# Performance work log

Hardware: AMD Instinct MI355X
Metric: run time of the kernel (lower is better)

Reference implementation:

```python
import jax, jax.numpy as jnp
import numpy as np

B, CQ, CKV, H, W = 8, 256, 512, 64, 64
HKV, WKV = 32, 32
DQK = CQ // 8  # 32


def setup_inputs() -> dict:
    key = jax.random.key(0)
    ks = jax.random.split(key, 9)
    s = 0.05
    return {
        "query": jax.random.normal(ks[0], (B, CQ, H, W), jnp.float32),
        "key_value": jax.random.normal(ks[1], (B, CKV, HKV, WKV), jnp.float32),
        "Wq": jax.random.normal(ks[2], (DQK, CQ), jnp.float32) * s,
        "bq": jax.random.normal(ks[3], (DQK,), jnp.float32) * s,
        "Wk": jax.random.normal(ks[4], (DQK, CKV), jnp.float32) * s,
        "bk": jax.random.normal(ks[5], (DQK,), jnp.float32) * s,
        "Wv": jax.random.normal(ks[6], (CQ, CKV), jnp.float32) * s,
        "bv": jax.random.normal(ks[7], (CQ,), jnp.float32) * s,
        "gamma": jax.random.normal(ks[8], (1,), jnp.float32) * 0.5,
    }


def reference(query, key_value, Wq, bq, Wk, bk, Wv, bv, gamma):
    b, cq, h, w = query.shape
    n = h * w
    # bilinear resize of key_value to query's spatial size (align_corners=False
    # half-pixel convention, matching torch F.interpolate and jax.image.resize)
    kv = jax.image.resize(key_value, (b, key_value.shape[1], h, w), method="bilinear")
    # 1x1 convs are channel contractions
    q = jnp.einsum("bchw,dc->bdhw", query, Wq) + bq[None, :, None, None]   # [B,DQK,H,W]
    k = jnp.einsum("bchw,dc->bdhw", kv, Wk) + bk[None, :, None, None]      # [B,DQK,H,W]
    v = jnp.einsum("bchw,dc->bdhw", kv, Wv) + bv[None, :, None, None]      # [B,CQ,H,W]
    qf = q.reshape(b, -1, n)   # [B,DQK,N]
    kf = k.reshape(b, -1, n)   # [B,DQK,N]
    vf = v.reshape(b, -1, n)   # [B,CQ,N]
    energy = jnp.einsum("bdn,bdm->bnm", qf, kf)        # [B,N,N]
    attention = jax.nn.softmax(energy, axis=-1)
    out = jnp.einsum("bnm,bcm->bcn", attention, vf)     # [B,CQ,N]
    out = out.reshape(b, cq, h, w)
    return gamma[0] * out + query
```

## Files before the change

### kernel.cpp

```cpp
#include <hip/hip_runtime.h>

#define B_ 8
#define CQ_ 256
#define CKV_ 512
#define N_ 4096
#define DQK_ 32

typedef __bf16 bf16;
typedef __bf16 bf16x4 __attribute__((ext_vector_type(4)));
typedef __bf16 bf16x8 __attribute__((ext_vector_type(8)));
typedef float f32x4 __attribute__((ext_vector_type(4)));

__global__ void k_convert_w(const float* __restrict__ Wq, const float* __restrict__ Wk,
                            const float* __restrict__ Wv,
                            bf16* __restrict__ wq, bf16* __restrict__ wk, bf16* __restrict__ wv) {
    int i = blockIdx.x * 256 + threadIdx.x;
    if (i < 8192) wq[i] = (bf16)Wq[i];
    else if (i < 24576) wk[i - 8192] = (bf16)Wk[i - 8192];
    else if (i < 155648) wv[i - 24576] = (bf16)Wv[i - 24576];
}

__global__ __launch_bounds__(256) void k_resize(const float* __restrict__ kv, bf16* __restrict__ kvr) {
    const int yo = blockIdx.x;
    const int b  = blockIdx.y;
    const int tid = threadIdx.x;
    __shared__ float r0[64][33];
    __shared__ float r1[64][33];
    int ty = yo >> 1;
    int y0, y1; float wy0, wy1;
    if ((yo & 1) == 0) { y0 = ty > 0 ? ty - 1 : 0; y1 = ty; wy0 = 0.25f; wy1 = 0.75f; }
    else               { y0 = ty; y1 = ty < 31 ? ty + 1 : 31; wy0 = 0.75f; wy1 = 0.25f; }
    const int u_loc = tid & 63;
    const int xo_base = tid >> 6;
    for (int uc = 0; uc < CKV_; uc += 64) {
        __syncthreads();
        for (int i = 0; i < 8; ++i) {
            int idx = tid + i * 256;
            int u = idx >> 5, x = idx & 31;
            const float* src = kv + ((size_t)b * CKV_ + uc + u) * 1024 + x;
            r0[u][x] = src[y0 * 32];
            r1[u][x] = src[y1 * 32];
        }
        __syncthreads();
        for (int i = 0; i < 16; ++i) {
            int xo = xo_base + i * 4;
            int tx = xo >> 1;
            int xa, xb; float wxa, wxb;
            if ((xo & 1) == 0) { xa = tx > 0 ? tx - 1 : 0; xb = tx; wxa = 0.25f; wxb = 0.75f; }
            else               { xa = tx; xb = tx < 31 ? tx + 1 : 31; wxa = 0.75f; wxb = 0.25f; }
            float v0 = wxa * r0[u_loc][xa] + wxb * r0[u_loc][xb];
            float v1 = wxa * r1[u_loc][xa] + wxb * r1[u_loc][xb];
            float val = wy0 * v0 + wy1 * v1;
            kvr[((size_t)b * N_ + yo * 64 + xo) * CKV_ + uc + u_loc] = (bf16)val;
        }
    }
}

__global__ __launch_bounds__(256) void k_proj_q_fused(const float* __restrict__ query,
                                                      const bf16* __restrict__ W,
                                                      const float* __restrict__ bias,
                                                      bf16* __restrict__ qTb) {
    __shared__ bf16 tile[64][264];
    const int n0 = blockIdx.x * 64;
    const int b  = blockIdx.y;
    const int tid = threadIdx.x;
    const int xi = tid & 15, c0 = tid >> 4;
    for (int pass = 0; pass < 16; ++pass) {
        int c = c0 + pass * 16;
        const float4 v = *(const float4*)(query + ((size_t)b * CQ_ + c) * N_ + n0 + xi * 4);
        tile[xi * 4 + 0][c] = (bf16)v.x;
        tile[xi * 4 + 1][c] = (bf16)v.y;
        tile[xi * 4 + 2][c] = (bf16)v.z;
        tile[xi * 4 + 3][c] = (bf16)v.w;
    }
    __syncthreads();
    const int w = tid >> 6, lane = tid & 63;
    const int l16 = lane & 15, quad = lane >> 4;
    const int ct = w & 1, nh = w >> 1;
    f32x4 acc[2];
    acc[0] = (f32x4){0.f, 0.f, 0.f, 0.f}; acc[1] = (f32x4){0.f, 0.f, 0.f, 0.f};
    const bf16* aptr = W + (ct * 16 + l16) * CQ_ + quad * 8;
#pragma unroll
    for (int ks = 0; ks < 8; ++ks) {
        bf16x8 af = *(const bf16x8*)(aptr + ks * 32);
        for (int j = 0; j < 2; ++j) {
            bf16x8 bfv = *(const bf16x8*)&tile[nh * 32 + j * 16 + l16][ks * 32 + quad * 8];
            acc[j] = __builtin_amdgcn_mfma_f32_16x16x32_bf16(af, bfv, acc[j], 0, 0, 0);
        }
    }
    for (int j = 0; j < 2; ++j)
        for (int r = 0; r < 4; ++r) {
            int d = ct * 16 + quad * 4 + r;
            int n = n0 + nh * 32 + j * 16 + l16;
            qTb[((size_t)b * N_ + n) * DQK_ + d] = (bf16)(acc[j][r] + bias[d]);
        }
}

__global__ __launch_bounds__(256) void k_proj_k(const bf16* __restrict__ W,
                                                const float* __restrict__ bias,
                                                const bf16* __restrict__ Bm,
                                                bf16* __restrict__ outT) {
    const int mb = blockIdx.x * 128;
    const int b  = blockIdx.y;
    const int tid = threadIdx.x;
    const int w = tid >> 6, lane = tid & 63;
    const int l16 = lane & 15, quad = lane >> 4;
    const int ct = w & 1;
    const int mhalf = (w >> 1) * 64;
    f32x4 acc[4];
    for (int j = 0; j < 4; ++j) acc[j] = (f32x4){0.f, 0.f, 0.f, 0.f};
    const bf16* aptr  = W + (ct * 16 + l16) * CKV_ + quad * 8;
    const bf16* bbase = Bm + ((size_t)b * N_ + mb + mhalf) * CKV_ + quad * 8;
#pragma unroll
    for (int ks = 0; ks < 16; ++ks) {
        bf16x8 af = *(const bf16x8*)(aptr + ks * 32);
        for (int j = 0; j < 4; ++j) {
            bf16x8 bfv = *(const bf16x8*)(bbase + (size_t)(j * 16 + l16) * CKV_ + ks * 32);
            acc[j] = __builtin_amdgcn_mfma_f32_16x16x32_bf16(af, bfv, acc[j], 0, 0, 0);
        }
    }
    for (int j = 0; j < 4; ++j)
        for (int r = 0; r < 4; ++r) {
            int d = ct * 16 + quad * 4 + r;
            int m = mb + mhalf + j * 16 + l16;
            outT[((size_t)b * N_ + m) * DQK_ + d] = (bf16)(acc[j][r] + bias[d]);
        }
}

__global__ __launch_bounds__(256) void k_proj_v(const bf16* __restrict__ W,
                                                const float* __restrict__ bias,
                                                const bf16* __restrict__ Bm,
                                                bf16* __restrict__ vout) {
    const int mb = blockIdx.x * 64;
    const int b  = blockIdx.y;
    const int tid = threadIdx.x;
    const int w = tid >> 6, lane = tid & 63;
    const int l16 = lane & 15, quad = lane >> 4;
    f32x4 acc[4][4];
    for (int i = 0; i < 4; ++i) for (int j = 0; j < 4; ++j) acc[i][j] = (f32x4){0.f, 0.f, 0.f, 0.f};
    const bf16* bbase = Bm + ((size_t)b * N_ + mb) * CKV_ + quad * 8;
#pragma unroll 4
    for (int ks = 0; ks < 16; ++ks) {
        bf16x8 bfv[4];
        for (int j = 0; j < 4; ++j)
            bfv[j] = *(const bf16x8*)(bbase + (size_t)(j * 16 + l16) * CKV_ + ks * 32);
        for (int i = 0; i < 4; ++i) {
            bf16x8 af = *(const bf16x8*)(W + (size_t)((w * 4 + i) * 16 + l16) * CKV_ + ks * 32 + quad * 8);
            for (int j = 0; j < 4; ++j)
                acc[i][j] = __builtin_amdgcn_mfma_f32_16x16x32_bf16(af, bfv[j], acc[i][j], 0, 0, 0);
        }
    }
    for (int i = 0; i < 4; ++i)
        for (int r = 0; r < 4; ++r) {
            int c = (w * 4 + i) * 16 + quad * 4 + r;
            float bvs = bias[c];
            for (int j = 0; j < 4; ++j) {
                int m = mb + j * 16 + l16;
                vout[((size_t)b * CQ_ + c) * N_ + m] = (bf16)(acc[i][j][r] + bvs);
            }
        }
}

__global__ __launch_bounds__(256) void k_flash(const bf16* __restrict__ qT,
                                               const bf16* __restrict__ kT,
                                               const bf16* __restrict__ vv,
                                               const float* __restrict__ query,
                                               const float* __restrict__ gamma,
                                               float* __restrict__ out) {
    __shared__ bf16 P[2][64][72];
    __shared__ float linvs[64];
    const int b  = blockIdx.y;
    const int n0 = blockIdx.x * 64;
    const int tid = threadIdx.x;
    const int w = tid >> 6, lane = tid & 63;
    const int l16 = lane & 15, quad = lane >> 4;
    const int swz = l16 & 3;

    const bf16x8 qfrag = *(const bf16x8*)(qT + ((size_t)b * N_ + n0 + w * 16 + l16) * DQK_ + quad * 8);

    f32x4 acc[4][4];
    for (int i = 0; i < 4; ++i) for (int j = 0; j < 4; ++j) acc[i][j] = (f32x4){0.f, 0.f, 0.f, 0.f};
    f32x4 lsum = (f32x4){0.f, 0.f, 0.f, 0.f};

    const bf16* kbase = kT + (size_t)b * N_ * DQK_;
    const bf16* vbase = vv + ((size_t)b * CQ_ + w * 64) * N_;

    bf16x8 kf[4];
    for (int im = 0; im < 4; ++im)
        kf[im] = *(const bf16x8*)(kbase + (size_t)(im * 16 + l16) * DQK_ + quad * 8);

    for (int mt = 0; mt < 64; ++mt) {
        const int m0 = mt * 64;
        bf16 (* __restrict__ Pb)[72] = P[mt & 1];
        for (int im = 0; im < 4; ++im) {
            f32x4 s = __builtin_amdgcn_mfma_f32_16x16x32_bf16(kf[im], qfrag,
                                                              (f32x4){0.f, 0.f, 0.f, 0.f}, 0, 0, 0);
            bf16x4 pk;
            for (int r = 0; r < 4; ++r) {
                float p = __expf(s[r]);
                lsum[r] += p;
                pk[r] = (bf16)p;
            }
            *(bf16x4*)&Pb[w * 16 + l16][((im ^ swz) << 4) + quad * 4] = pk;
        }
        bf16x8 vf[2][4];
        for (int ks = 0; ks < 2; ++ks)
            for (int i = 0; i < 4; ++i)
                vf[ks][i] = *(const bf16x8*)(vbase + (size_t)(i * 16 + l16) * N_ + m0 + ks * 32 + quad * 8);
        const int m1 = (mt + 1 < 64 ? mt + 1 : 0) * 64;
        bf16x8 kn[4];
        for (int im = 0; im < 4; ++im)
            kn[im] = *(const bf16x8*)(kbase + (size_t)(m1 + im * 16 + l16) * DQK_ + quad * 8);
        __syncthreads();
        for (int ks = 0; ks < 2; ++ks) {
            bf16x8 pf[4];
            for (int j = 0; j < 4; ++j)
                pf[j] = *(const bf16x8*)&Pb[j * 16 + l16]
                            [((((ks << 1) | (quad >> 1)) ^ swz) << 4) + ((quad & 1) << 3)];
            for (int i = 0; i < 4; ++i)
                for (int j = 0; j < 4; ++j)
                    acc[i][j] = __builtin_amdgcn_mfma_f32_16x16x32_bf16(vf[ks][i], pf[j], acc[i][j], 0, 0, 0);
        }
        for (int im = 0; im < 4; ++im) kf[im] = kn[im];
    }
    float s = (lsum[0] + lsum[1]) + (lsum[2] + lsum[3]);
    s += __shfl_xor(s, 16);
    s += __shfl_xor(s, 32);
    if (quad == 0) linvs[w * 16 + l16] = 1.f / s;
    __syncthreads();
    float linv[4];
    for (int j = 0; j < 4; ++j) linv[j] = linvs[j * 16 + l16];
    const float g = gamma[0];
    for (int i = 0; i < 4; ++i)
        for (int r = 0; r < 4; ++r) {
            int c = w * 64 + i * 16 + quad * 4 + r;
            for (int j = 0; j < 4; ++j) {
                int n = n0 + j * 16 + l16;
                size_t idx = ((size_t)b * CQ_ + c) * N_ + n;
                out[idx] = g * acc[i][j][r] * linv[j] + query[idx];
            }
        }
}

extern "C" void kernel_launch(void* const* d_in, const int* in_sizes, int n_in,
                              void* d_out, int out_size, void* d_ws, size_t ws_size,
                              hipStream_t stream) {
    const float* query     = (const float*)d_in[0];
    const float* key_value = (const float*)d_in[1];
    const float* Wq = (const float*)d_in[2];
    const float* bq = (const float*)d_in[3];
    const float* Wk = (const float*)d_in[4];
    const float* bk = (const float*)d_in[5];
    const float* Wv = (const float*)d_in[6];
    const float* bv = (const float*)d_in[7];
    const float* gamma = (const float*)d_in[8];
    float* out = (float*)d_out;

    char* ws = (char*)d_ws;
    bf16* kvr  = (bf16*)(ws);
    bf16* vbuf = (bf16*)(ws + 33554432);
    bf16* qTb  = (bf16*)(ws + 50331648);
    bf16* kTb  = (bf16*)(ws + 52428800);
    bf16* wqb  = (bf16*)(ws + 54525952);
    bf16* wkb  = (bf16*)(ws + 54542336);
    bf16* wvb  = (bf16*)(ws + 54575104);

    k_convert_w<<<608, 256, 0, stream>>>(Wq, Wk, Wv, wqb, wkb, wvb);
    k_resize<<<dim3(64, 8), 256, 0, stream>>>(key_value, kvr);
    k_proj_q_fused<<<dim3(64, 8), 256, 0, stream>>>(query, wqb, bq, qTb);
    k_proj_k<<<dim3(32, 8), 256, 0, stream>>>(wkb, bk, kvr, kTb);
    k_proj_v<<<dim3(64, 8), 256, 0, stream>>>(wvb, bv, kvr, vbuf);
    k_flash<<<dim3(64, 8), 256, 0, stream>>>(qTb, kTb, vbuf, query, gamma, out);
}
```

Baseline: 341.8 us.

## Software-pipeline attention loop: compute next tile's scores while accumulating current PV

Restructures the flash-attention main loop into a prologue, a steady state and an epilogue. In the steady state each iteration computes the exp scores for tile t+1 into the alternate LDS buffer while running the PV MFMAs for tile t, and K is prefetched two tiles ahead. The goal is to overlap exp/VALU work with matrix-core work and to move the barrier to the end of the iteration. This costs some register pressure and duplicated epilogue code.

```diff
diff --git a/kernel.cpp b/kernel.cpp
--- a/kernel.cpp
+++ b/kernel.cpp
@@ -185,15 +185,13 @@
     const bf16* kbase = kT + (size_t)b * N_ * DQK_;
     const bf16* vbase = vv + ((size_t)b * CQ_ + w * 64) * N_;
 
-    bf16x8 kf[4];
-    for (int im = 0; im < 4; ++im)
-        kf[im] = *(const bf16x8*)(kbase + (size_t)(im * 16 + l16) * DQK_ + quad * 8);
-
-    for (int mt = 0; mt < 64; ++mt) {
-        const int m0 = mt * 64;
-        bf16 (* __restrict__ Pb)[72] = P[mt & 1];
+    auto loadK = [&](int mt, bf16x8* dst) {
+        for (int im = 0; im < 4; ++im)
+            dst[im] = *(const bf16x8*)(kbase + (size_t)(mt * 64 + im * 16 + l16) * DQK_ + quad * 8);
+    };
+    auto computeS = [&](const bf16x8* kfr, bf16 (*Pb)[72]) {
         for (int im = 0; im < 4; ++im) {
-            f32x4 s = __builtin_amdgcn_mfma_f32_16x16x32_bf16(kf[im], qfrag,
+            f32x4 s = __builtin_amdgcn_mfma_f32_16x16x32_bf16(kfr[im], qfrag,
                                                               (f32x4){0.f, 0.f, 0.f, 0.f}, 0, 0, 0);
             bf16x4 pk;
             for (int r = 0; r < 4; ++r) {
@@ -203,15 +201,24 @@
             }
             *(bf16x4*)&Pb[w * 16 + l16][((im ^ swz) << 4) + quad * 4] = pk;
         }
+    };
+
+    bf16x8 kf[4];
+    loadK(0, kf);
+    computeS(kf, P[0]);
+    loadK(1, kf);
+    __syncthreads();
+
+    for (int t = 0; t < 63; ++t) {
+        const int m0 = t * 64;
         bf16x8 vf[2][4];
         for (int ks = 0; ks < 2; ++ks)
             for (int i = 0; i < 4; ++i)
                 vf[ks][i] = *(const bf16x8*)(vbase + (size_t)(i * 16 + l16) * N_ + m0 + ks * 32 + quad * 8);
-        const int m1 = (mt + 1 < 64 ? mt + 1 : 0) * 64;
         bf16x8 kn[4];
-        for (int im = 0; im < 4; ++im)
-            kn[im] = *(const bf16x8*)(kbase + (size_t)(m1 + im * 16 + l16) * DQK_ + quad * 8);
-        __syncthreads();
+        loadK(t + 2 < 64 ? t + 2 : 0, kn);
+        computeS(kf, P[(t + 1) & 1]);
+        bf16 (* __restrict__ Pb)[72] = P[t & 1];
         for (int ks = 0; ks < 2; ++ks) {
             bf16x8 pf[4];
             for (int j = 0; j < 4; ++j)
@@ -222,6 +229,24 @@
                     acc[i][j] = __builtin_amdgcn_mfma_f32_16x16x32_bf16(vf[ks][i], pf[j], acc[i][j], 0, 0, 0);
         }
         for (int im = 0; im < 4; ++im) kf[im] = kn[im];
+        __syncthreads();
+    }
+    {
+        const int m0 = 63 * 64;
+        bf16x8 vf[2][4];
+        for (int ks = 0; ks < 2; ++ks)
+            for (int i = 0; i < 4; ++i)
+                vf[ks][i] = *(const bf16x8*)(vbase + (size_t)(i * 16 + l16) * N_ + m0 + ks * 32 + quad * 8);
+        bf16 (* __restrict__ Pb)[72] = P[1];
+        for (int ks = 0; ks < 2; ++ks) {
+            bf16x8 pf[4];
+            for (int j = 0; j < 4; ++j)
+                pf[j] = *(const bf16x8*)&Pb[j * 16 + l16]
+                            [((((ks << 1) | (quad >> 1)) ^ swz) << 4) + ((quad & 1) << 3)];
+            for (int i = 0; i < 4; ++i)
+                for (int j = 0; j < 4; ++j)
+                    acc[i][j] = __builtin_amdgcn_mfma_f32_16x16x32_bf16(vf[ks][i], pf[j], acc[i][j], 0, 0, 0);
+        }
     }
     float s = (lsum[0] + lsum[1]) + (lsum[2] + lsum[3]);
     s += __shfl_xor(s, 16);
```

After: 342.5 us. About the same (+0.2%).

## Make flash attention warp-independent with per-wave P tiles and software pipelining

Applied to the files above, without the earlier changes.

Each wave now owns its own 16 query rows and computes all 256 output channels, so P lives in per-wave double-buffered LDS and the block-wide __syncthreads in the main loop is removed. The loop is software-pipelined: the next tile's S/exp is computed while the current tile's P feeds the PV MFMAs. The block-to-(batch, query-tile) mapping is also interleaved across batches. In exchange, every wave loads the full V tile, which raises V global/L2 traffic fourfold per block, and the accumulator grows to 16 fragments per wave, adding register pressure.

```diff
diff --git a/kernel.cpp b/kernel.cpp
--- a/kernel.cpp
+++ b/kernel.cpp
@@ -167,33 +167,35 @@
                                                const float* __restrict__ query,
                                                const float* __restrict__ gamma,
                                                float* __restrict__ out) {
-    __shared__ bf16 P[2][64][72];
-    __shared__ float linvs[64];
-    const int b  = blockIdx.y;
-    const int n0 = blockIdx.x * 64;
-    const int tid = threadIdx.x;
-    const int w = tid >> 6, lane = tid & 63;
-    const int l16 = lane & 15, quad = lane >> 4;
-    const int swz = l16 & 3;
+    __shared__ bf16 P[4][2][16][64];
+    const int tid = threadIdx.x;
+    const int w = tid >> 6, lane = tid & 63;
+    const int l16 = lane & 15, quad = lane >> 4;
+    const int swz = (l16 & 7) << 3;
+    const int flat = blockIdx.x + 64 * blockIdx.y;
+    const int b  = flat & 7;
+    const int n0 = (flat >> 3) * 64;
 
     const bf16x8 qfrag = *(const bf16x8*)(qT + ((size_t)b * N_ + n0 + w * 16 + l16) * DQK_ + quad * 8);
 
-    f32x4 acc[4][4];
-    for (int i = 0; i < 4; ++i) for (int j = 0; j < 4; ++j) acc[i][j] = (f32x4){0.f, 0.f, 0.f, 0.f};
+    f32x4 acc[16];
+#pragma unroll
+    for (int i = 0; i < 16; ++i) acc[i] = (f32x4){0.f, 0.f, 0.f, 0.f};
     f32x4 lsum = (f32x4){0.f, 0.f, 0.f, 0.f};
 
     const bf16* kbase = kT + (size_t)b * N_ * DQK_;
-    const bf16* vbase = vv + ((size_t)b * CQ_ + w * 64) * N_;
-
-    bf16x8 kf[4];
-    for (int im = 0; im < 4; ++im)
-        kf[im] = *(const bf16x8*)(kbase + (size_t)(im * 16 + l16) * DQK_ + quad * 8);
-
-    for (int mt = 0; mt < 64; ++mt) {
-        const int m0 = mt * 64;
-        bf16 (* __restrict__ Pb)[72] = P[mt & 1];
+    const bf16* vbase = vv + (size_t)b * CQ_ * N_ + (size_t)l16 * N_ + quad * 8;
+
+    bf16* const Pw0 = &P[w][0][0][0];
+    bf16* const Pw1 = &P[w][1][0][0];
+
+    auto loadK = [&](int mt, bf16x8* dst) {
+        for (int im = 0; im < 4; ++im)
+            dst[im] = *(const bf16x8*)(kbase + (size_t)(mt * 64 + im * 16 + l16) * DQK_ + quad * 8);
+    };
+    auto computeS = [&](const bf16x8* kfr, bf16* Pb) {
         for (int im = 0; im < 4; ++im) {
-            f32x4 s = __builtin_amdgcn_mfma_f32_16x16x32_bf16(kf[im], qfrag,
+            f32x4 s = __builtin_amdgcn_mfma_f32_16x16x32_bf16(kfr[im], qfrag,
                                                               (f32x4){0.f, 0.f, 0.f, 0.f}, 0, 0, 0);
             bf16x4 pk;
             for (int r = 0; r < 4; ++r) {
@@ -201,44 +203,60 @@
                 lsum[r] += p;
                 pk[r] = (bf16)p;
             }
-            *(bf16x4*)&Pb[w * 16 + l16][((im ^ swz) << 4) + quad * 4] = pk;
-        }
-        bf16x8 vf[2][4];
-        for (int ks = 0; ks < 2; ++ks)
-            for (int i = 0; i < 4; ++i)
-                vf[ks][i] = *(const bf16x8*)(vbase + (size_t)(i * 16 + l16) * N_ + m0 + ks * 32 + quad * 8);
-        const int m1 = (mt + 1 < 64 ? mt + 1 : 0) * 64;
+            *(bf16x4*)&Pb[l16 * 64 + ((im * 16 + quad * 4) ^ swz)] = pk;
+        }
+    };
+
+    bf16x8 kf[4];
+    loadK(0, kf);
+    computeS(kf, Pw0);
+    loadK(1, kf);
+
+    const int roff0 = l16 * 64 + ((quad * 8) ^ swz);
+    const int roff1 = l16 * 64 + ((32 + quad * 8) ^ swz);
+
+    for (int t = 0; t < 63; ++t) {
+        bf16* Pr = (t & 1) ? Pw1 : Pw0;
+        bf16* Pwr = (t & 1) ? Pw0 : Pw1;
+        bf16x8 pf0 = *(const bf16x8*)&Pr[roff0];
+        bf16x8 pf1 = *(const bf16x8*)&Pr[roff1];
+        computeS(kf, Pwr);
         bf16x8 kn[4];
-        for (int im = 0; im < 4; ++im)
-            kn[im] = *(const bf16x8*)(kbase + (size_t)(m1 + im * 16 + l16) * DQK_ + quad * 8);
-        __syncthreads();
-        for (int ks = 0; ks < 2; ++ks) {
-            bf16x8 pf[4];
-            for (int j = 0; j < 4; ++j)
-                pf[j] = *(const bf16x8*)&Pb[j * 16 + l16]
-                            [((((ks << 1) | (quad >> 1)) ^ swz) << 4) + ((quad & 1) << 3)];
-            for (int i = 0; i < 4; ++i)
-                for (int j = 0; j < 4; ++j)
-                    acc[i][j] = __builtin_amdgcn_mfma_f32_16x16x32_bf16(vf[ks][i], pf[j], acc[i][j], 0, 0, 0);
+        loadK(t + 2 < 64 ? t + 2 : 0, kn);
+        const bf16* vp = vbase + t * 64;
+#pragma unroll
+        for (int i = 0; i < 16; ++i) {
+            bf16x8 v0 = *(const bf16x8*)(vp + (size_t)i * (16 * N_));
+            bf16x8 v1 = *(const bf16x8*)(vp + (size_t)i * (16 * N_) + 32);
+            acc[i] = __builtin_amdgcn_mfma_f32_16x16x32_bf16(v0, pf0, acc[i], 0, 0, 0);
+            acc[i] = __builtin_amdgcn_mfma_f32_16x16x32_bf16(v1, pf1, acc[i], 0, 0, 0);
         }
         for (int im = 0; im < 4; ++im) kf[im] = kn[im];
+    }
+    {
+        bf16x8 pf0 = *(const bf16x8*)&Pw1[roff0];
+        bf16x8 pf1 = *(const bf16x8*)&Pw1[roff1];
+        const bf16* vp = vbase + 63 * 64;
+#pragma unroll
+        for (int i = 0; i < 16; ++i) {
+            bf16x8 v0 = *(const bf16x8*)(vp + (size_t)i * (16 * N_));
+            bf16x8 v1 = *(const bf16x8*)(vp + (size_t)i * (16 * N_) + 32);
+            acc[i] = __builtin_amdgcn_mfma_f32_16x16x32_bf16(v0, pf0, acc[i], 0, 0, 0);
+            acc[i] = __builtin_amdgcn_mfma_f32_16x16x32_bf16(v1, pf1, acc[i], 0, 0, 0);
+        }
     }
     float s = (lsum[0] + lsum[1]) + (lsum[2] + lsum[3]);
     s += __shfl_xor(s, 16);
     s += __shfl_xor(s, 32);
-    if (quad == 0) linvs[w * 16 + l16] = 1.f / s;
-    __syncthreads();
-    float linv[4];
-    for (int j = 0; j < 4; ++j) linv[j] = linvs[j * 16 + l16];
+    const float linv = 1.f / s;
     const float g = gamma[0];
-    for (int i = 0; i < 4; ++i)
-        for (int r = 0; r < 4; ++r) {
-            int c = w * 64 + i * 16 + quad * 4 + r;
-            for (int j = 0; j < 4; ++j) {
-                int n = n0 + j * 16 + l16;
-                size_t idx = ((size_t)b * CQ_ + c) * N_ + n;
-                out[idx] = g * acc[i][j][r] * linv[j] + query[idx];
-            }
+    const int n = n0 + w * 16 + l16;
+#pragma unroll
+    for (int i = 0; i < 16; ++i)
+        for (int r = 0; r < 4; ++r) {
+            int c = i * 16 + quad * 4 + r;
+            size_t idx = ((size_t)b * CQ_ + c) * N_ + n;
+            out[idx] = g * acc[i][r] * linv + query[idx];
         }
 }
 
```

Result: slower. 687.6 us (+101.1%).
